# Kernel optimization log

Measured on AMD Instinct MI355X. Metric: run time of the kernel, lower is better.

The kernel has to match this reference:

```python
import jax, jax.numpy as jnp
import numpy as np

SCALE = 2
GROUPS = 4


def _init_pos(scale, groups, dtype=jnp.float32):
    # h = arange((-s+1)/2, (s-1)/2 + 1) / s
    h = (jnp.arange(scale, dtype=dtype) - (scale - 1) / 2) / scale
    yy, xx = jnp.meshgrid(h, h, indexing='ij')
    pos = jnp.stack([xx, yy], axis=0)              # [2, s, s]
    # torch .repeat(1, groups, 1, 1) tiles along the size-2 dim -> [2*G, s, s]
    return jnp.tile(pos, (groups, 1, 1)).reshape(1, -1, 1, 1)  # [1, 2*G*s*s, 1, 1]


def _pixel_shuffle(x, r):
    B, C, H, W = x.shape
    Co = C // (r * r)
    x = x.reshape(B, Co, r, r, H, W)
    x = x.transpose(0, 1, 4, 2, 5, 3)              # [B, Co, H, r, W, r]
    return x.reshape(B, Co, H * r, W * r)


def _grid_sample_border(img, grid):
    # img: [N, C, H, W]; grid: [N, Ho, Wo, 2] in [-1, 1] (x, y); bilinear,
    # align_corners=False, padding_mode='border' (coords clamped first).
    N, C, H, W = img.shape
    gx, gy = grid[..., 0], grid[..., 1]
    ix = jnp.clip(((gx + 1) * W - 1) * 0.5, 0.0, W - 1)
    iy = jnp.clip(((gy + 1) * H - 1) * 0.5, 0.0, H - 1)
    x0f = jnp.floor(ix); y0f = jnp.floor(iy)
    wx = (ix - x0f)[:, None]                       # [N, 1, Ho, Wo]
    wy = (iy - y0f)[:, None]
    x0 = x0f.astype(jnp.int32); y0 = y0f.astype(jnp.int32)
    x1 = jnp.minimum(x0 + 1, W - 1); y1 = jnp.minimum(y0 + 1, H - 1)

    def gather(im, y, x):                          # im [C,H,W], y/x [Ho,Wo]
        return im[:, y, x]                         # [C, Ho, Wo]
    gv = jax.vmap(gather)

    return ((1 - wy) * ((1 - wx) * gv(img, y0, x0) + wx * gv(img, y0, x1))
            + wy * ((1 - wx) * gv(img, y1, x0) + wx * gv(img, y1, x1)))


def setup_inputs() -> dict:
    key = jax.random.key(0)
    k1, k2 = jax.random.split(key)
    B, C, H, W = 16, 64, 128, 128
    out_ch = 2 * GROUPS * SCALE ** 2               # 32
    x = jax.random.normal(k1, (B, C, H, W), dtype=jnp.float32)
    w_off = jax.random.normal(k2, (out_ch, C), dtype=jnp.float32) * 0.001
    b_off = jnp.zeros((out_ch,), dtype=jnp.float32)
    return {"x": x, "w_off": w_off, "b_off": b_off}


def reference(x, w_off, b_off):
    B, C, H, W = x.shape
    s, G = SCALE, GROUPS
    # 1x1 conv offset, scaled by 0.25, plus fixed sub-pixel init positions
    offset = jnp.einsum('bchw,oc->bohw', x, w_off) + b_off[None, :, None, None]
    offset = offset * 0.25 + _init_pos(s, G, x.dtype)   # [B, 2*G*s*s, H, W]

    off = offset.reshape(B, 2, G * s * s, H, W)
    cx = jnp.arange(W, dtype=x.dtype) + 0.5
    cy = jnp.arange(H, dtype=x.dtype) + 0.5
    yy, xx = jnp.meshgrid(cy, cx, indexing='ij')
    coords = jnp.stack([xx, yy], axis=0)[None, :, None]  # [1, 2, 1, H, W]
    norm = jnp.array([W, H], dtype=x.dtype).reshape(1, 2, 1, 1, 1)
    coords = 2 * (coords + off) / norm - 1               # [B, 2, G*s*s, H, W]

    coords = _pixel_shuffle(coords.reshape(B, 2 * G * s * s, H, W), s)  # [B, 2G, sH, sW]
    grid = coords.reshape(B, 2, G, s * H, s * W)
    grid = grid.transpose(0, 2, 3, 4, 1).reshape(B * G, s * H, s * W, 2)

    out = _grid_sample_border(x.reshape(B * G, C // G, H, W), grid)
    return out.reshape(B, C, s * H, s * W)
```

## Files before the change

### kernel.cpp

```cpp
#include <hip/hip_runtime.h>
#include <hip/hip_fp16.h>


namespace {
constexpr int CC = 64;
constexpr int HH = 128;
constexpr int WW = 128;
constexpr int HW = HH * WW;
constexpr int OW = 2 * WW;
constexpr int OHW = 4 * HW;
constexpr int TH = 8, TW = 32;
typedef float vfloat2 __attribute__((ext_vector_type(2)));
}

__global__ __launch_bounds__(256, 8)
void dysample_kernel(const float* __restrict__ x,
                     const float* __restrict__ w_off,
                     const float* __restrict__ b_off,
                     float* __restrict__ out) {
    __shared__ __half2 offh[8][256];

    const int tid = threadIdx.x;
    const int gg   = blockIdx.x & 1;
    const int tile = (blockIdx.x >> 1) & 63;
    const int b    = blockIdx.x >> 7;
    const int th0  = (tile >> 2) * TH;
    const int tw0  = (tile & 3) * TW;
    const int ty   = tid >> 5;
    const int tx   = tid & 31;
    const int h    = th0 + ty;
    const int w    = tw0 + tx;
    const int q0   = gg * 8;

    float accx[8], accy[8];
#pragma unroll
    for (int j = 0; j < 8; ++j) {
        accx[j] = b_off[q0 + j];
        accy[j] = b_off[q0 + j + 16];
    }

    const float* xb = x + b * (CC * HW) + h * WW + w;
#pragma unroll
    for (int chunk = 0; chunk < 4; ++chunk) {
        float xv[16];
#pragma unroll
        for (int c = 0; c < 16; ++c) xv[c] = xb[(chunk * 16 + c) * HW];
#pragma unroll
        for (int j = 0; j < 8; ++j) {
            float ax = accx[j], ay = accy[j];
            const float* wx_ = w_off + (q0 + j) * 64 + chunk * 16;
            const float* wy_ = wx_ + 16 * 64;
#pragma unroll
            for (int c = 0; c < 16; ++c) ax = fmaf(xv[c], wx_[c], ax);
#pragma unroll
            for (int c = 0; c < 16; ++c) ay = fmaf(xv[c], wy_[c], ay);
            accx[j] = ax; accy[j] = ay;
        }
    }

#pragma unroll
    for (int j = 0; j < 8; ++j) {
        const int q = q0 + j, g = q >> 2, r1 = (q >> 1) & 1, r2 = q & 1;
        const float init = (((g & 1) ? r1 : r2) ? 0.25f : -0.25f);
        const float offx = fmaf(accx[j], 0.25f, init);
        const float offy = fmaf(accy[j], 0.25f, init);
        offh[j][tid] = __floats2half2_rn(offx, offy);
    }
    __syncthreads();

    const int k   = tid & 31;
    const float fw = (float)(tw0 + k);
#pragma unroll
    for (int gi = 0; gi < 2; ++gi) {
        const int g = gg * 2 + gi;
        const float* xg = x + (b * CC + g * 16) * HW;
        float* og = out + (size_t)(b * CC + g * 16) * OHW;
#pragma unroll
        for (int rep = 0; rep < 2; ++rep) {
            const int oy  = rep * 8 + (ty);
            const int jq  = gi * 4 + ((oy & 1) << 1);
            const int pix = ((oy >> 1) << 5) | k;
            const float2 o0 = __half22float2(offh[jq][pix]);
            const float2 o1 = __half22float2(offh[jq + 1][pix]);
            const float fh = (float)(th0 + (oy >> 1));

            float ix0 = ((fw + 0.5f) + o0.x) - 0.5f;
            float iy0 = ((fh + 0.5f) + o0.y) - 0.5f;
            float ix1 = ((fw + 0.5f) + o1.x) - 0.5f;
            float iy1 = ((fh + 0.5f) + o1.y) - 0.5f;
            ix0 = fminf(fmaxf(ix0, 0.0f), 127.0f);
            iy0 = fminf(fmaxf(iy0, 0.0f), 127.0f);
            ix1 = fminf(fmaxf(ix1, 0.0f), 127.0f);
            iy1 = fminf(fmaxf(iy1, 0.0f), 127.0f);

            const float x0f0 = floorf(ix0), y0f0 = floorf(iy0);
            const float x0f1 = floorf(ix1), y0f1 = floorf(iy1);
            const float wx0 = ix0 - x0f0, wy0 = iy0 - y0f0;
            const float wx1 = ix1 - x0f1, wy1 = iy1 - y0f1;
            const int xa0 = (int)x0f0, ya0 = (int)y0f0;
            const int xa1 = (int)x0f1, ya1 = (int)y0f1;
            const int xb0 = min(xa0 + 1, WW - 1), yb0 = min(ya0 + 1, HH - 1);
            const int xb1 = min(xa1 + 1, WW - 1), yb1 = min(ya1 + 1, HH - 1);
            const int a00 = ya0 * WW + xa0, a01 = ya0 * WW + xb0;
            const int a10 = yb0 * WW + xa0, a11 = yb0 * WW + xb0;
            const int b00 = ya1 * WW + xa1, b01 = ya1 * WW + xb1;
            const int b10 = yb1 * WW + xa1, b11 = yb1 * WW + xb1;
            const int oidx = (th0 * 2 + oy) * OW + (tw0 * 2 + 2 * k);

#pragma unroll
            for (int c = 0; c < 16; ++c) {
                const float* xs = xg + c * HW;
                const float va00 = xs[a00], va01 = xs[a01];
                const float va10 = xs[a10], va11 = xs[a11];
                const float vb00 = xs[b00], vb01 = xs[b01];
                const float vb10 = xs[b10], vb11 = xs[b11];
                const float t0 = fmaf(wx0, va01 - va00, va00);
                const float u0 = fmaf(wx0, va11 - va10, va10);
                const float t1 = fmaf(wx1, vb01 - vb00, vb00);
                const float u1 = fmaf(wx1, vb11 - vb10, vb10);
                vfloat2 r;
                r.x = fmaf(wy0, u0 - t0, t0);
                r.y = fmaf(wy1, u1 - t1, t1);
                __builtin_nontemporal_store(r, (vfloat2*)(og + c * OHW + oidx));
            }
        }
    }
}

extern "C" void kernel_launch(void* const* d_in, const int* in_sizes, int n_in,
                              void* d_out, int out_size, void* d_ws, size_t ws_size,
                              hipStream_t stream) {
    const float* x     = (const float*)d_in[0];
    const float* w_off = (const float*)d_in[1];
    const float* b_off = (const float*)d_in[2];
    float* out = (float*)d_out;
    (void)in_sizes; (void)n_in; (void)out_size; (void)d_ws; (void)ws_size;
    dysample_kernel<<<dim3(16 * 64 * 2), dim3(256), 0, stream>>>(x, w_off, b_off, out);
}
```

Measured before the change: 384.6 us.

## Stage haloed input window in LDS and vectorize grid-sample output stores

```diff
diff --git a/kernel.cpp b/kernel.cpp
--- a/kernel.cpp
+++ b/kernel.cpp
@@ -10,7 +10,10 @@
 constexpr int OW = 2 * WW;
 constexpr int OHW = 4 * HW;
 constexpr int TH = 8, TW = 32;
-typedef float vfloat2 __attribute__((ext_vector_type(2)));
+constexpr int WR = 10, WC = 34, WS = 36;
+constexpr int WPLANE = WR * WS;
+constexpr int WELEMS = WR * WC;
+typedef float vfloat4 __attribute__((ext_vector_type(4)));
 }
 
 __global__ __launch_bounds__(256, 8)
@@ -19,6 +22,7 @@
                      const float* __restrict__ b_off,
                      float* __restrict__ out) {
     __shared__ __half2 offh[8][256];
+    __shared__ float win[2][2][WPLANE];
 
     const int tid = threadIdx.x;
     const int gg   = blockIdx.x & 1;
@@ -26,104 +30,183 @@
     const int b    = blockIdx.x >> 7;
     const int th0  = (tile >> 2) * TH;
     const int tw0  = (tile & 3) * TW;
-    const int ty   = tid >> 5;
-    const int tx   = tid & 31;
-    const int h    = th0 + ty;
-    const int w    = tw0 + tx;
-    const int q0   = gg * 8;
-
-    float accx[8], accy[8];
-#pragma unroll
-    for (int j = 0; j < 8; ++j) {
-        accx[j] = b_off[q0 + j];
-        accy[j] = b_off[q0 + j + 16];
-    }
-
-    const float* xb = x + b * (CC * HW) + h * WW + w;
-#pragma unroll
-    for (int chunk = 0; chunk < 4; ++chunk) {
-        float xv[16];
-#pragma unroll
-        for (int c = 0; c < 16; ++c) xv[c] = xb[(chunk * 16 + c) * HW];
+
+    {
+        const int ty = tid >> 5;
+        const int tx = tid & 31;
+        const int h  = th0 + ty;
+        const int w  = tw0 + tx;
+        const int q0 = gg * 8;
+
+        float accx[8], accy[8];
 #pragma unroll
         for (int j = 0; j < 8; ++j) {
-            float ax = accx[j], ay = accy[j];
-            const float* wx_ = w_off + (q0 + j) * 64 + chunk * 16;
-            const float* wy_ = wx_ + 16 * 64;
-#pragma unroll
-            for (int c = 0; c < 16; ++c) ax = fmaf(xv[c], wx_[c], ax);
-#pragma unroll
-            for (int c = 0; c < 16; ++c) ay = fmaf(xv[c], wy_[c], ay);
-            accx[j] = ax; accy[j] = ay;
-        }
-    }
-
-#pragma unroll
-    for (int j = 0; j < 8; ++j) {
-        const int q = q0 + j, g = q >> 2, r1 = (q >> 1) & 1, r2 = q & 1;
-        const float init = (((g & 1) ? r1 : r2) ? 0.25f : -0.25f);
-        const float offx = fmaf(accx[j], 0.25f, init);
-        const float offy = fmaf(accy[j], 0.25f, init);
-        offh[j][tid] = __floats2half2_rn(offx, offy);
+            accx[j] = b_off[q0 + j];
+            accy[j] = b_off[q0 + j + 16];
+        }
+
+        const float* xb = x + b * (CC * HW) + h * WW + w;
+#pragma unroll
+        for (int chunk = 0; chunk < 4; ++chunk) {
+            float xv[16];
+#pragma unroll
+            for (int c = 0; c < 16; ++c) xv[c] = xb[(chunk * 16 + c) * HW];
+#pragma unroll
+            for (int j = 0; j < 8; ++j) {
+                float ax = accx[j], ay = accy[j];
+                const float* wx_ = w_off + (q0 + j) * 64 + chunk * 16;
+                const float* wy_ = wx_ + 16 * 64;
+#pragma unroll
+                for (int c = 0; c < 16; ++c) ax = fmaf(xv[c], wx_[c], ax);
+#pragma unroll
+                for (int c = 0; c < 16; ++c) ay = fmaf(xv[c], wy_[c], ay);
+                accx[j] = ax; accy[j] = ay;
+            }
+        }
+
+#pragma unroll
+        for (int j = 0; j < 8; ++j) {
+            const int q = q0 + j, g = q >> 2, r1_ = (q >> 1) & 1, r2_ = q & 1;
+            const float init = (((g & 1) ? r1_ : r2_) ? 0.25f : -0.25f);
+            const float offx = fmaf(accx[j], 0.25f, init);
+            const float offy = fmaf(accy[j], 0.25f, init);
+            offh[j][tid] = __floats2half2_rn(offx, offy);
+        }
     }
     __syncthreads();
 
-    const int k   = tid & 31;
-    const float fw = (float)(tw0 + k);
+    const int oy  = tid >> 4;
+    const int ox4 = tid & 15;
+    const int hl  = oy >> 1;
+    const int r1  = oy & 1;
+
+    float wxv[8], wyv[8];
+    int aidx[8];
+    bool valid = true;
 #pragma unroll
     for (int gi = 0; gi < 2; ++gi) {
-        const int g = gg * 2 + gi;
-        const float* xg = x + (b * CC + g * 16) * HW;
-        float* og = out + (size_t)(b * CC + g * 16) * OHW;
-#pragma unroll
-        for (int rep = 0; rep < 2; ++rep) {
-            const int oy  = rep * 8 + (ty);
-            const int jq  = gi * 4 + ((oy & 1) << 1);
-            const int pix = ((oy >> 1) << 5) | k;
-            const float2 o0 = __half22float2(offh[jq][pix]);
-            const float2 o1 = __half22float2(offh[jq + 1][pix]);
-            const float fh = (float)(th0 + (oy >> 1));
-
-            float ix0 = ((fw + 0.5f) + o0.x) - 0.5f;
-            float iy0 = ((fh + 0.5f) + o0.y) - 0.5f;
-            float ix1 = ((fw + 0.5f) + o1.x) - 0.5f;
-            float iy1 = ((fh + 0.5f) + o1.y) - 0.5f;
-            ix0 = fminf(fmaxf(ix0, 0.0f), 127.0f);
-            iy0 = fminf(fmaxf(iy0, 0.0f), 127.0f);
-            ix1 = fminf(fmaxf(ix1, 0.0f), 127.0f);
-            iy1 = fminf(fmaxf(iy1, 0.0f), 127.0f);
-
-            const float x0f0 = floorf(ix0), y0f0 = floorf(iy0);
-            const float x0f1 = floorf(ix1), y0f1 = floorf(iy1);
-            const float wx0 = ix0 - x0f0, wy0 = iy0 - y0f0;
-            const float wx1 = ix1 - x0f1, wy1 = iy1 - y0f1;
-            const int xa0 = (int)x0f0, ya0 = (int)y0f0;
-            const int xa1 = (int)x0f1, ya1 = (int)y0f1;
-            const int xb0 = min(xa0 + 1, WW - 1), yb0 = min(ya0 + 1, HH - 1);
-            const int xb1 = min(xa1 + 1, WW - 1), yb1 = min(ya1 + 1, HH - 1);
-            const int a00 = ya0 * WW + xa0, a01 = ya0 * WW + xb0;
-            const int a10 = yb0 * WW + xa0, a11 = yb0 * WW + xb0;
-            const int b00 = ya1 * WW + xa1, b01 = ya1 * WW + xb1;
-            const int b10 = yb1 * WW + xa1, b11 = yb1 * WW + xb1;
-            const int oidx = (th0 * 2 + oy) * OW + (tw0 * 2 + 2 * k);
-
-#pragma unroll
-            for (int c = 0; c < 16; ++c) {
-                const float* xs = xg + c * HW;
-                const float va00 = xs[a00], va01 = xs[a01];
-                const float va10 = xs[a10], va11 = xs[a11];
-                const float vb00 = xs[b00], vb01 = xs[b01];
-                const float vb10 = xs[b10], vb11 = xs[b11];
-                const float t0 = fmaf(wx0, va01 - va00, va00);
-                const float u0 = fmaf(wx0, va11 - va10, va10);
-                const float t1 = fmaf(wx1, vb01 - vb00, vb00);
-                const float u1 = fmaf(wx1, vb11 - vb10, vb10);
-                vfloat2 r;
-                r.x = fmaf(wy0, u0 - t0, t0);
-                r.y = fmaf(wy1, u1 - t1, t1);
-                __builtin_nontemporal_store(r, (vfloat2*)(og + c * OHW + oidx));
+#pragma unroll
+        for (int pp = 0; pp < 4; ++pp) {
+            const int s8 = gi * 4 + pp;
+            const int wl = 2 * ox4 + (pp >> 1);
+            const int j  = gi * 4 + (r1 << 1) + (pp & 1);
+            const float2 o = __half22float2(offh[j][hl * 32 + wl]);
+            float ix = ((float)(tw0 + wl) + 0.5f + o.x) - 0.5f;
+            float iy = ((float)(th0 + hl) + 0.5f + o.y) - 0.5f;
+            ix = fminf(fmaxf(ix, 0.0f), 127.0f);
+            iy = fminf(fmaxf(iy, 0.0f), 127.0f);
+            const float x0f = floorf(ix), y0f = floorf(iy);
+            wxv[s8] = ix - x0f;
+            wyv[s8] = iy - y0f;
+            const int wi = (int)x0f - (tw0 - 1);
+            const int ri = (int)y0f - (th0 - 1);
+            valid = valid && ((unsigned)wi <= 32u) && ((unsigned)ri <= 8u);
+            aidx[s8] = ri * WS + wi;
+        }
+    }
+
+    const float* xbase = x + (size_t)(b * CC + gg * 32) * HW;
+    int soff0 = 0, soff1 = 0, soff2 = 0, dst0 = 0, dst1 = 0, dst2 = 0;
+#pragma unroll
+    for (int k = 0; k < 3; ++k) {
+        const int e = tid + 256 * k;
+        const int p = (e >= WELEMS) ? 1 : 0;
+        const int rem = e - WELEMS * p;
+        const int r  = rem / WC;
+        const int jc = rem - r * WC;
+        const int gr = min(max(th0 - 1 + r, 0), HH - 1);
+        const int gc = min(max(tw0 - 1 + jc, 0), WW - 1);
+        const int so = p * 16 * HW + gr * WW + gc;
+        const int di = p * WPLANE + r * WS + jc;
+        if (k == 0)      { soff0 = so; dst0 = di; }
+        else if (k == 1) { soff1 = so; dst1 = di; }
+        else             { soff2 = so; dst2 = di; }
+    }
+    const bool has2 = (tid < 2 * WELEMS - 512);
+    float* const winf = &win[0][0][0];
+    float* const ob0 = out + (size_t)(b * CC + gg * 32) * OHW
+                     + (size_t)(2 * th0 + oy) * OW + 2 * tw0 + 4 * ox4;
+
+    {
+        const float s0 = xbase[soff0];
+        const float s1 = xbase[soff1];
+        float s2 = 0.0f;
+        if (has2) s2 = xbase[soff2];
+        winf[dst0] = s0;
+        winf[dst1] = s1;
+        if (has2) winf[dst2] = s2;
+        soff0 += HW; soff1 += HW; soff2 += HW;
+    }
+    __syncthreads();
+
+#pragma unroll 2
+    for (int c = 0; c < 16; ++c) {
+        const int buf = c & 1;
+        const bool more = (c < 15);
+        float s0 = 0.0f, s1 = 0.0f, s2 = 0.0f;
+        if (more) {
+            s0 = xbase[soff0];
+            s1 = xbase[soff1];
+            if (has2) s2 = xbase[soff2];
+            soff0 += HW; soff1 += HW; soff2 += HW;
+        }
+
+        const float* Wb = winf + buf * (2 * WPLANE);
+        if (valid) {
+#pragma unroll
+            for (int gi = 0; gi < 2; ++gi) {
+                const float* Wp = Wb + gi * WPLANE;
+                vfloat4 res;
+#pragma unroll
+                for (int pp = 0; pp < 4; ++pp) {
+                    const int s8 = gi * 4 + pp;
+                    const int a = aidx[s8];
+                    const float t00 = Wp[a],      t01 = Wp[a + 1];
+                    const float t10 = Wp[a + WS], t11 = Wp[a + WS + 1];
+                    const float hh0 = fmaf(wxv[s8], t01 - t00, t00);
+                    const float hh1 = fmaf(wxv[s8], t11 - t10, t10);
+                    res[pp] = fmaf(wyv[s8], hh1 - hh0, hh0);
+                }
+                __builtin_nontemporal_store(
+                    res, (vfloat4*)(ob0 + (size_t)(gi * 16 + c) * OHW));
             }
-        }
+        } else {
+#pragma unroll
+            for (int gi = 0; gi < 2; ++gi) {
+                vfloat4 res;
+#pragma unroll
+                for (int pp = 0; pp < 4; ++pp) {
+                    const int wl = 2 * ox4 + (pp >> 1);
+                    const int j  = gi * 4 + (r1 << 1) + (pp & 1);
+                    const float2 o = __half22float2(offh[j][hl * 32 + wl]);
+                    float ix = ((float)(tw0 + wl) + 0.5f + o.x) - 0.5f;
+                    float iy = ((float)(th0 + hl) + 0.5f + o.y) - 0.5f;
+                    ix = fminf(fmaxf(ix, 0.0f), 127.0f);
+                    iy = fminf(fmaxf(iy, 0.0f), 127.0f);
+                    const float x0f = floorf(ix), y0f = floorf(iy);
+                    const float wx = ix - x0f, wy = iy - y0f;
+                    const int xa = (int)x0f, ya = (int)y0f;
+                    const int xb2 = min(xa + 1, WW - 1);
+                    const int yb2 = min(ya + 1, HH - 1);
+                    const float* xs = xbase + (size_t)(gi * 16 + c) * HW;
+                    const float v00 = xs[ya * WW + xa],  v01 = xs[ya * WW + xb2];
+                    const float v10 = xs[yb2 * WW + xa], v11 = xs[yb2 * WW + xb2];
+                    const float hh0 = fmaf(wx, v01 - v00, v00);
+                    const float hh1 = fmaf(wx, v11 - v10, v10);
+                    res[pp] = fmaf(wy, hh1 - hh0, hh0);
+                }
+                __builtin_nontemporal_store(
+                    res, (vfloat4*)(ob0 + (size_t)(gi * 16 + c) * OHW));
+            }
+        }
+
+        if (more) {
+            float* Wn = winf + (buf ^ 1) * (2 * WPLANE);
+            Wn[dst0] = s0;
+            Wn[dst1] = s1;
+            if (has2) Wn[dst2] = s2;
+        }
+        __syncthreads();
     }
 }
 
```

After: 464.6 us. 20.8% more time.

## Gather a 3x3 neighborhood once per pixel and reuse across four subpixel samples

Applied to the files above, without the earlier changes.

```diff
diff --git a/kernel.cpp b/kernel.cpp
--- a/kernel.cpp
+++ b/kernel.cpp
@@ -20,10 +20,11 @@
                      float* __restrict__ out) {
     __shared__ __half2 offh[8][256];
 
-    const int tid = threadIdx.x;
-    const int gg   = blockIdx.x & 1;
-    const int tile = (blockIdx.x >> 1) & 63;
-    const int b    = blockIdx.x >> 7;
+    const int tid  = threadIdx.x;
+    const int gg   = blockIdx.x >> 10;
+    const int rest = blockIdx.x & 1023;
+    const int tile = rest & 63;
+    const int b    = rest >> 6;
     const int th0  = (tile >> 2) * TH;
     const int tw0  = (tile & 3) * TW;
     const int ty   = tid >> 5;
@@ -32,96 +33,133 @@
     const int w    = tw0 + tx;
     const int q0   = gg * 8;
 
-    float accx[8], accy[8];
-#pragma unroll
-    for (int j = 0; j < 8; ++j) {
-        accx[j] = b_off[q0 + j];
-        accy[j] = b_off[q0 + j + 16];
-    }
-
-    const float* xb = x + b * (CC * HW) + h * WW + w;
-#pragma unroll
-    for (int chunk = 0; chunk < 4; ++chunk) {
-        float xv[16];
-#pragma unroll
-        for (int c = 0; c < 16; ++c) xv[c] = xb[(chunk * 16 + c) * HW];
+    {
+        float accx[8], accy[8];
 #pragma unroll
         for (int j = 0; j < 8; ++j) {
-            float ax = accx[j], ay = accy[j];
-            const float* wx_ = w_off + (q0 + j) * 64 + chunk * 16;
-            const float* wy_ = wx_ + 16 * 64;
+            accx[j] = b_off[q0 + j];
+            accy[j] = b_off[q0 + j + 16];
+        }
+
+        const float* xb = x + b * (CC * HW) + h * WW + w;
 #pragma unroll
-            for (int c = 0; c < 16; ++c) ax = fmaf(xv[c], wx_[c], ax);
+        for (int chunk = 0; chunk < 4; ++chunk) {
+            float xv[16];
 #pragma unroll
-            for (int c = 0; c < 16; ++c) ay = fmaf(xv[c], wy_[c], ay);
-            accx[j] = ax; accy[j] = ay;
+            for (int c = 0; c < 16; ++c) xv[c] = xb[(chunk * 16 + c) * HW];
+#pragma unroll
+            for (int j = 0; j < 8; ++j) {
+                float ax = accx[j], ay = accy[j];
+                const float* wx_ = w_off + (q0 + j) * 64 + chunk * 16;
+                const float* wy_ = wx_ + 16 * 64;
+#pragma unroll
+                for (int c = 0; c < 16; ++c) ax = fmaf(xv[c], wx_[c], ax);
+#pragma unroll
+                for (int c = 0; c < 16; ++c) ay = fmaf(xv[c], wy_[c], ay);
+                accx[j] = ax; accy[j] = ay;
+            }
         }
-    }
 
 #pragma unroll
-    for (int j = 0; j < 8; ++j) {
-        const int q = q0 + j, g = q >> 2, r1 = (q >> 1) & 1, r2 = q & 1;
-        const float init = (((g & 1) ? r1 : r2) ? 0.25f : -0.25f);
-        const float offx = fmaf(accx[j], 0.25f, init);
-        const float offy = fmaf(accy[j], 0.25f, init);
-        offh[j][tid] = __floats2half2_rn(offx, offy);
+        for (int j = 0; j < 8; ++j) {
+            const int q = q0 + j, g = q >> 2, r1_ = (q >> 1) & 1, r2_ = q & 1;
+            const float init = (((g & 1) ? r1_ : r2_) ? 0.25f : -0.25f);
+            const float offx = fmaf(accx[j], 0.25f, init);
+            const float offy = fmaf(accy[j], 0.25f, init);
+            offh[j][tid] = __floats2half2_rn(offx, offy);
+        }
     }
     __syncthreads();
 
-    const int k   = tid & 31;
-    const float fw = (float)(tw0 + k);
+    const int rm  = max(h - 1, 0) * WW;
+    const int r0_ = h * WW;
+    const int rp  = min(h + 1, HH - 1) * WW;
+    const int cm  = max(w - 1, 0);
+    const int cp  = min(w + 1, WW - 1);
+    const int a0 = rm + cm,  a1 = rm + w,  a2 = rm + cp;
+    const int a3 = r0_ + cm, a4 = r0_ + w, a5 = r0_ + cp;
+    const int a6 = rp + cm,  a7 = rp + w,  a8 = rp + cp;
+    const float fw = (float)w, fh = (float)h;
+
+    const float* xgg = x + (size_t)(b * CC + gg * 32) * HW;
+    float* ogg = out + (size_t)(b * CC + gg * 32) * OHW
+               + (size_t)(2 * h) * OW + 2 * w;
+
 #pragma unroll
     for (int gi = 0; gi < 2; ++gi) {
-        const int g = gg * 2 + gi;
-        const float* xg = x + (b * CC + g * 16) * HW;
-        float* og = out + (size_t)(b * CC + g * 16) * OHW;
+        float wcq[4][3], wrq[4][3];
+        bool vall = true;
 #pragma unroll
-        for (int rep = 0; rep < 2; ++rep) {
-            const int oy  = rep * 8 + (ty);
-            const int jq  = gi * 4 + ((oy & 1) << 1);
-            const int pix = ((oy >> 1) << 5) | k;
-            const float2 o0 = __half22float2(offh[jq][pix]);
-            const float2 o1 = __half22float2(offh[jq + 1][pix]);
-            const float fh = (float)(th0 + (oy >> 1));
+        for (int p = 0; p < 4; ++p) {
+            const float2 o = __half22float2(offh[gi * 4 + p][tid]);
+            float ix = ((fw + 0.5f) + o.x) - 0.5f;
+            float iy = ((fh + 0.5f) + o.y) - 0.5f;
+            ix = fminf(fmaxf(ix, 0.0f), 127.0f);
+            iy = fminf(fmaxf(iy, 0.0f), 127.0f);
+            const float x0f = floorf(ix), y0f = floorf(iy);
+            const float wx = ix - x0f, wy = iy - y0f;
+            const int sx = (int)x0f - (w - 1);
+            const int sy = (int)y0f - (h - 1);
+            vall = vall && ((unsigned)sx <= 1u) && ((unsigned)sy <= 1u);
+            const bool bx = (sx != 0), by = (sy != 0);
+            wcq[p][0] = bx ? 0.0f : 1.0f - wx;
+            wcq[p][1] = bx ? 1.0f - wx : wx;
+            wcq[p][2] = bx ? wx : 0.0f;
+            wrq[p][0] = by ? 0.0f : 1.0f - wy;
+            wrq[p][1] = by ? 1.0f - wy : wy;
+            wrq[p][2] = by ? wy : 0.0f;
+        }
 
-            float ix0 = ((fw + 0.5f) + o0.x) - 0.5f;
-            float iy0 = ((fh + 0.5f) + o0.y) - 0.5f;
-            float ix1 = ((fw + 0.5f) + o1.x) - 0.5f;
-            float iy1 = ((fh + 0.5f) + o1.y) - 0.5f;
-            ix0 = fminf(fmaxf(ix0, 0.0f), 127.0f);
-            iy0 = fminf(fmaxf(iy0, 0.0f), 127.0f);
-            ix1 = fminf(fmaxf(ix1, 0.0f), 127.0f);
-            iy1 = fminf(fmaxf(iy1, 0.0f), 127.0f);
+        const float* xg = xgg + (size_t)(gi * 16) * HW;
+        float* og = ogg + (size_t)(gi * 16) * OHW;
 
-            const float x0f0 = floorf(ix0), y0f0 = floorf(iy0);
-            const float x0f1 = floorf(ix1), y0f1 = floorf(iy1);
-            const float wx0 = ix0 - x0f0, wy0 = iy0 - y0f0;
-            const float wx1 = ix1 - x0f1, wy1 = iy1 - y0f1;
-            const int xa0 = (int)x0f0, ya0 = (int)y0f0;
-            const int xa1 = (int)x0f1, ya1 = (int)y0f1;
-            const int xb0 = min(xa0 + 1, WW - 1), yb0 = min(ya0 + 1, HH - 1);
-            const int xb1 = min(xa1 + 1, WW - 1), yb1 = min(ya1 + 1, HH - 1);
-            const int a00 = ya0 * WW + xa0, a01 = ya0 * WW + xb0;
-            const int a10 = yb0 * WW + xa0, a11 = yb0 * WW + xb0;
-            const int b00 = ya1 * WW + xa1, b01 = ya1 * WW + xb1;
-            const int b10 = yb1 * WW + xa1, b11 = yb1 * WW + xb1;
-            const int oidx = (th0 * 2 + oy) * OW + (tw0 * 2 + 2 * k);
-
-#pragma unroll
+        if (vall) {
+#pragma unroll 2
             for (int c = 0; c < 16; ++c) {
                 const float* xs = xg + c * HW;
-                const float va00 = xs[a00], va01 = xs[a01];
-                const float va10 = xs[a10], va11 = xs[a11];
-                const float vb00 = xs[b00], vb01 = xs[b01];
-                const float vb10 = xs[b10], vb11 = xs[b11];
-                const float t0 = fmaf(wx0, va01 - va00, va00);
-                const float u0 = fmaf(wx0, va11 - va10, va10);
-                const float t1 = fmaf(wx1, vb01 - vb00, vb00);
-                const float u1 = fmaf(wx1, vb11 - vb10, vb10);
-                vfloat2 r;
-                r.x = fmaf(wy0, u0 - t0, t0);
-                r.y = fmaf(wy1, u1 - t1, t1);
-                __builtin_nontemporal_store(r, (vfloat2*)(og + c * OHW + oidx));
+                const float m0 = xs[a0], m1 = xs[a1], m2 = xs[a2];
+                const float m3 = xs[a3], m4 = xs[a4], m5 = xs[a5];
+                const float m6 = xs[a6], m7 = xs[a7], m8 = xs[a8];
+                float res[4];
+#pragma unroll
+                for (int p = 0; p < 4; ++p) {
+                    const float rd0 = fmaf(wcq[p][2], m2,
+                                      fmaf(wcq[p][1], m1, wcq[p][0] * m0));
+                    const float rd1 = fmaf(wcq[p][2], m5,
+                                      fmaf(wcq[p][1], m4, wcq[p][0] * m3));
+                    const float rd2 = fmaf(wcq[p][2], m8,
+                                      fmaf(wcq[p][1], m7, wcq[p][0] * m6));
+                    res[p] = fmaf(wrq[p][2], rd2,
+                             fmaf(wrq[p][1], rd1, wrq[p][0] * rd0));
+                }
+                vfloat2 lo, hi;
+                lo.x = res[0]; lo.y = res[1];
+                hi.x = res[2]; hi.y = res[3];
+                *(vfloat2*)(og + (size_t)c * OHW) = lo;
+                *(vfloat2*)(og + (size_t)c * OHW + OW) = hi;
+            }
+        } else {
+            for (int c = 0; c < 16; ++c) {
+                const float* xs = xg + c * HW;
+#pragma unroll
+                for (int p = 0; p < 4; ++p) {
+                    const float2 o = __half22float2(offh[gi * 4 + p][tid]);
+                    float ix = ((fw + 0.5f) + o.x) - 0.5f;
+                    float iy = ((fh + 0.5f) + o.y) - 0.5f;
+                    ix = fminf(fmaxf(ix, 0.0f), 127.0f);
+                    iy = fminf(fmaxf(iy, 0.0f), 127.0f);
+                    const float x0f = floorf(ix), y0f = floorf(iy);
+                    const float wx = ix - x0f, wy = iy - y0f;
+                    const int xa = (int)x0f, ya = (int)y0f;
+                    const int xb2 = min(xa + 1, WW - 1);
+                    const int yb2 = min(ya + 1, HH - 1);
+                    const float v00 = xs[ya * WW + xa],  v01 = xs[ya * WW + xb2];
+                    const float v10 = xs[yb2 * WW + xa], v11 = xs[yb2 * WW + xb2];
+                    const float t = fmaf(wx, v01 - v00, v00);
+                    const float u = fmaf(wx, v11 - v10, v10);
+                    og[(size_t)c * OHW + (size_t)(p >> 1) * OW + (p & 1)] =
+                        fmaf(wy, u - t, t);
+                }
             }
         }
     }
@@ -135,5 +173,5 @@
     const float* b_off = (const float*)d_in[2];
     float* out = (float*)d_out;
     (void)in_sizes; (void)n_in; (void)out_size; (void)d_ws; (void)ws_size;
-    dysample_kernel<<<dim3(16 * 64 * 2), dim3(256), 0, stream>>>(x, w_off, b_off, out);
+    dysample_kernel<<<dim3(2048), dim3(256), 0, stream>>>(x, w_off, b_off, out);
 }
```

Result: slower. 553.3 us (+43.9%).
